# Kernel tuning notes

Measured on AMD Instinct MI355X. Metric: run time of the kernel, lower is better.

## Reference

```python
import jax, jax.numpy as jnp
import numpy as np

# dims
B, NO, NE = 32, 100, 600          # batch, img objects, img edges
NK, KE, L = 1000, 1000, 8         # kg entities, kg edges, token len
R = 8                              # reasoning-program nodes
H, IMG, LOC = 512, 2048, 5        # hidden, img feat, loc feat
EMB, V, MID, C = 300, 10000, 512, 3000
PAD = 1


def lang_encode(tokens, embed, W, b):
    # masked mean-pool of word embeddings + projection (LanguageEncoder)
    m = (tokens != PAD).astype(jnp.float32)            # [B,N,L]
    e = embed[tokens]                                   # [B,N,L,EMB]
    pooled = (e * m[..., None]).sum(-2) / jnp.maximum(m.sum(-1, keepdims=True), 1.0)
    return jnp.tanh(pooled @ W + b)                     # [B,N,H]


def find_attn(q, k, mask, Wq, Wk, v):
    # Find module: additive attention of program-node queries over key set
    qp = q @ Wq                                         # [B,R,MID]
    kp = k @ Wk                                         # [B,N,MID]
    s = jnp.einsum('brnm,m->brn', jnp.tanh(qp[:, :, None, :] + kp[:, None, :, :]), v)
    if mask is not None:
        s = jnp.where(mask[:, None, :], s, -1e9)
    return jax.nn.softmax(s, axis=-1)                   # [B,R,N] attention maps


def setup_inputs():
    key = jax.random.key(0)
    ks = jax.random.split(key, 30)
    w = lambda i, shp: jax.random.normal(ks[i], shp, jnp.float32) * 0.05
    inp = {
        'img_feat': jax.random.normal(ks[0], (B, NO, IMG), jnp.float32),
        'img_loc': jax.random.uniform(ks[1], (B, NO, LOC), jnp.float32),
        'img_node1_id_list': jax.random.randint(ks[2], (B, NE), 0, NO),
        'img_node2_id_list': jax.random.randint(ks[3], (B, NE), 0, NO),
        'kg_entity': jax.random.randint(ks[4], (B, NK, L), 0, V),
        'kg_e1_ids_list': jax.random.randint(ks[5], (B, KE), 0, NK),
        'kg_e2_ids_list': jax.random.randint(ks[6], (B, KE), 0, NK),
        'kg_edge': jax.random.randint(ks[7], (B, KE, L), 0, V),
        'r_nodes': jax.random.randint(ks[8], (B, R, L), 0, V),
        'r_connects': jax.random.randint(ks[9], (B, R), 0, R),
        'r_type': jax.random.randint(ks[10], (B, R), 0, 3),
        'embed': w(11, (V, EMB)),
        'W_lang': w(12, (EMB, H)), 'b_lang': jnp.zeros((H,), jnp.float32),
        'W_img': w(13, (IMG, H)), 'b_img': jnp.zeros((H,), jnp.float32),
        'W_loc': w(14, (LOC, H)), 'b_loc': jnp.zeros((H,), jnp.float32),
        'W_rel': w(15, (2 * H, H)), 'b_rel': jnp.zeros((H,), jnp.float32),
        'Wq_n': w(16, (H, MID)), 'Wk_n': w(17, (H, MID)), 'v_n': w(18, (MID,)),
        'Wq_e': w(19, (H, MID)), 'Wk_e': w(20, (H, MID)), 'v_e': w(21, (MID,)),
        'W1': w(22, (H, MID)), 'b1': jnp.zeros((MID,), jnp.float32),
        'W2': w(23, (MID, C)), 'b2': jnp.zeros((C,), jnp.float32),
    }
    return inp


def reference(img_feat, img_loc, img_node1_id_list, img_node2_id_list, kg_entity,
              kg_e1_ids_list, kg_e2_ids_list, kg_edge, r_nodes, r_connects, r_type,
              embed, W_lang, b_lang, W_img, b_img, W_loc, b_loc, W_rel, b_rel,
              Wq_n, Wk_n, v_n, Wq_e, Wk_e, v_e, W1, b1, W2, b2):
    # --- image graph features ---
    img_f = img_feat @ W_img + b_img                    # [B,NO,H]
    img_node_feat = img_f + (img_loc @ W_loc + b_loc)
    n1 = jnp.take_along_axis(img_f, img_node1_id_list[..., None], axis=1)  # [B,NE,H]
    n2 = jnp.take_along_axis(img_f, img_node2_id_list[..., None], axis=1)
    img_edge_feat = jnp.concatenate([n1, n2], -1) @ W_rel + b_rel          # [B,NE,H]
    # --- kg graph features ---
    kg_node_feat = lang_encode(kg_entity, embed, W_lang, b_lang)           # [B,NK,H]
    kg_node_mask = jnp.any(kg_entity != PAD, axis=-1)                      # [B,NK]
    kg_edge_feat = lang_encode(kg_edge, embed, W_lang, b_lang)             # [B,KE,H]
    # --- reasoning-program node features ---
    r_feat = lang_encode(r_nodes, embed, W_lang, b_lang)                   # [B,R,H]
    # --- Find over nodes (img + kg entities) ---
    node_keys = jnp.concatenate([img_node_feat, kg_node_feat], axis=1)     # [B,NO+NK,H]
    node_mask = jnp.concatenate([jnp.ones((B, NO), bool), kg_node_mask], axis=1)
    all_map = find_attn(r_feat, node_keys, node_mask, Wq_n, Wk_n, v_n)     # [B,R,NO+NK]
    node_re = jnp.einsum('brn,bnh->brh', all_map, node_keys)               # grounded node feats
    # --- Find over edges (img + kg relations) ---
    edge_keys = jnp.concatenate([img_edge_feat, kg_edge_feat], axis=1)     # [B,NE+KE,H]
    edge_map = find_attn(r_feat, edge_keys, None, Wq_e, Wk_e, v_e)
    edge_ctx = jnp.einsum('brn,bnh->brh', edge_map, edge_keys)
    # --- Reason head on root program node ---
    final = node_re[:, -1] + edge_ctx[:, -1]                               # [B,H]
    return jnp.tanh(final @ W1 + b1) @ W2 + b2                             # [B,C]
```

## Files before the change

kernel.cpp:

```cpp
#include <hip/hip_runtime.h>
#include <hip/hip_bf16.h>
#include <math.h>

#define B_   32
#define NO_  100
#define NE_  600
#define NK_  1000
#define KE_  1000
#define L_   8
#define R_   8
#define H_   512
#define IMG_ 2048
#define LOC_ 5
#define EMB_ 300
#define MID_ 512
#define C_   3000
#define PAD_ 1

#define NN_  (NO_ + NK_)
#define NEK_ (NE_ + KE_)

typedef __attribute__((ext_vector_type(8))) short bf16x8;
typedef __attribute__((ext_vector_type(4))) float f32x4;

__device__ __forceinline__ float4 ldf4(const float* p) { return *(const float4*)p; }

__device__ __forceinline__ float bf2f(short s) {
    unsigned u = ((unsigned)(unsigned short)s) << 16;
    float f; __builtin_memcpy(&f, &u, 4); return f;
}
__device__ __forceinline__ short f2bf(float f) {
    unsigned u; __builtin_memcpy(&u, &f, 4);
    u = (u + 0x7fffu + ((u >> 16) & 1u)) >> 16;
    return (short)u;
}

__device__ __forceinline__ void gload16(const void* g, void* l) {
    __builtin_amdgcn_global_load_lds(
        (__attribute__((address_space(1))) void*)(g),
        (__attribute__((address_space(3))) void*)(l), 16, 0, 0);
}

__global__ __launch_bounds__(256) void wprep_kernel(
    const float* __restrict__ W, short* __restrict__ Wp, int K, int KS)
{
    int idx = blockIdx.x * 256 + threadIdx.x;
    int total = 4 * KS * 4 * 128;
    if (idx >= total) return;
    int nl = idx & 127;
    int kg = (idx >> 7) & 3;
    int t  = idx >> 9;
    int ks = t % KS;
    int nb = t / KS;
    int n = nb * 128 + nl;
    short o[8];
#pragma unroll
    for (int j = 0; j < 8; ++j) {
        int k = ks * 32 + kg * 8 + j;
        o[j] = (k < K) ? f2bf(W[(long)k * H_ + n]) : (short)0;
    }
    *(uint4*)&Wp[(long)idx * 8] = *(uint4*)o;
}

__global__ __launch_bounds__(256) void cvt_bf16_kernel(
    const float* __restrict__ src, short* __restrict__ dst, long n)
{
    long i = ((long)blockIdx.x * 256 + threadIdx.x) * 8;
    if (i >= n) return;
    float4 a = ldf4(src + i), b = ldf4(src + i + 4);
    short o[8] = { f2bf(a.x), f2bf(a.y), f2bf(a.z), f2bf(a.w),
                   f2bf(b.x), f2bf(b.y), f2bf(b.z), f2bf(b.w) };
    *(uint4*)&dst[i] = *(uint4*)o;
}

__global__ __launch_bounds__(256) void pool_kernel(
    const int* __restrict__ tokens, int tok_stride, int tok_off,
    const short* __restrict__ embed_bf, short* __restrict__ pooled,
    float* __restrict__ maskout, int nrows)
{
    __shared__ int   toks[32][8];
    __shared__ float rinv[32];
    int tid = threadIdx.x, base = blockIdx.x * 32;
    {
        int r = tid >> 3, t = tid & 7;
        int i = base + r;
        toks[r][t] = (i < nrows) ? tokens[tok_off + (long)i * tok_stride + t] : PAD_;
    }
    __syncthreads();
    if (tid < 32) {
        int c = 0;
#pragma unroll
        for (int t = 0; t < 8; ++t) c += (toks[tid][t] != PAD_);
        rinv[tid] = 1.0f / fmaxf((float)c, 1.0f);
        int i = base + tid;
        if (maskout && i < nrows) maskout[i] = (c > 0) ? 1.0f : 0.0f;
    }
    __syncthreads();

    for (int task = tid; task < 32 * 40; task += 256) {
        int r = task / 40, kg = task - r * 40;
        float s[8] = {0.f,0.f,0.f,0.f,0.f,0.f,0.f,0.f};
        if (kg < 38) {
#pragma unroll
            for (int t = 0; t < 8; ++t) {
                int tok = toks[r][t];
                if (tok != PAD_) {
                    bf16x8 e = *(const bf16x8*)&embed_bf[(long)tok * EMB_ + kg * 8];
#pragma unroll
                    for (int j = 0; j < 8; ++j) s[j] += bf2f(e[j]);
                }
            }
        }
        float iv = rinv[r];
        short o[8];
#pragma unroll
        for (int j = 0; j < 8; ++j) {
            float v = s[j] * iv;
            if (kg == 37 && j >= 4) v = 0.f;
            o[j] = f2bf(v);
        }
        *(uint4*)&pooled[(long)(base + r) * 320 + kg * 8] = *(uint4*)o;
    }
}

template<int OUTF32>
__global__ __launch_bounds__(256) void keys_gemm_kernel(
    const short* __restrict__ A, const short* __restrict__ Wp,
    const float* __restrict__ bias,
    void* __restrict__ out, int rows_per_b, long out_bstride, long out_roff,
    int nrows)
{
    const int KS = 10;
    __shared__ __align__(16) short As[2 * 4096];
    __shared__ __align__(16) short Bs[2 * 4096];
    int tid = threadIdx.x;
    int m0 = blockIdx.x * 128, nb = blockIdx.y, n0 = nb * 128;
    int w = tid >> 6, l = tid & 63, wr = w >> 1, wc = w & 1;
    const short* wslab = Wp + (long)nb * KS * 4096;

    auto stage = [&](int buf, int ks) {
        short* Ad = As + buf * 4096 + w * 1024;
        short* Bd = Bs + buf * 4096 + w * 1024;
        const short* bsrc = wslab + (long)ks * 4096 + w * 1024 + l * 8;
#pragma unroll
        for (int i = 0; i < 2; ++i) {
            const short* ga = A + (long)(m0 + i * 64 + l) * 320 + ks * 32 + w * 8;
            gload16(ga, Ad + i * 512);
            gload16(bsrc + i * 512, Bd + i * 512);
        }
    };

    f32x4 acc[4][4];
#pragma unroll
    for (int m = 0; m < 4; ++m)
#pragma unroll
        for (int n = 0; n < 4; ++n)
#pragma unroll
            for (int k = 0; k < 4; ++k) acc[m][n][k] = 0.f;

    int kg = l >> 4, li = l & 15;
    stage(0, 0);
    __syncthreads();
    int buf = 0;
    for (int ks = 0; ks < KS; ++ks) {
        if (ks + 1 < KS) stage(buf ^ 1, ks + 1);
        bf16x8 af[4], bfr[4];
#pragma unroll
        for (int m = 0; m < 4; ++m)
            af[m] = *(const bf16x8*)&As[buf * 4096 + kg * 1024 + (wr * 64 + m * 16 + li) * 8];
#pragma unroll
        for (int n = 0; n < 4; ++n)
            bfr[n] = *(const bf16x8*)&Bs[buf * 4096 + kg * 1024 + (wc * 64 + n * 16 + li) * 8];
#pragma unroll
        for (int m = 0; m < 4; ++m)
#pragma unroll
            for (int n = 0; n < 4; ++n)
                acc[m][n] = __builtin_amdgcn_mfma_f32_16x16x32_bf16(af[m], bfr[n], acc[m][n], 0, 0, 0);
        __syncthreads();
        buf ^= 1;
    }

    int jrow4 = (l >> 4) * 4;
    float bv[4];
#pragma unroll
    for (int n = 0; n < 4; ++n) bv[n] = bias[n0 + wc * 64 + n * 16 + li];
#pragma unroll
    for (int m = 0; m < 4; ++m)
#pragma unroll
        for (int j = 0; j < 4; ++j) {
            int i = m0 + wr * 64 + m * 16 + jrow4 + j;
            if (i >= nrows) continue;
            int b = i / rows_per_b, k = i - b * rows_per_b;
#pragma unroll
            for (int n = 0; n < 4; ++n) {
                int col = n0 + wc * 64 + n * 16 + li;
                float val = tanhf(acc[m][n][j] + bv[n]);
                long idx = (long)b * out_bstride + out_roff + (long)k * H_ + col;
                if (OUTF32) ((float*)out)[idx] = val;
                else        ((short*)out)[idx] = f2bf(val);
            }
        }
}

template<int AV, int EP, int KS>
__global__ __launch_bounds__(256) void mfma_gemm_kernel(
    const short* __restrict__ A, int lda, const short* __restrict__ Wp,
    const int* __restrict__ id1, const int* __restrict__ id2,
    const short* __restrict__ Agather,
    const float* __restrict__ bias, const float* __restrict__ bias2,
    const float* __restrict__ loc, const float* __restrict__ Wloc,
    const float* __restrict__ qp, const float* __restrict__ vvec,
    short* __restrict__ out0, short* __restrict__ out1,
    float* __restrict__ sout, int Nrows, int Mtot)
{
    __shared__ __align__(16) short As[2 * 4096];
    __shared__ __align__(16) short Bs[2 * 4096];
    int tid = threadIdx.x;
    int m0 = blockIdx.x * 128, nb = blockIdx.y, n0 = nb * 128;
    int w = tid >> 6, l = tid & 63, wr = w >> 1, wc = w & 1;

    int r1[2], r2[2];
    if (AV == 2) {
#pragma unroll
        for (int i = 0; i < 2; ++i) {
            int row = m0 + i * 64 + l;
            int b = row / NE_;
            r1[i] = b * NO_ + id1[row];
            r2[i] = b * NO_ + id2[row];
        }
    }
    const short* wslab = Wp + (long)nb * KS * 4096;

    auto stage = [&](int buf, int ks) {
        short* Ad = As + buf * 4096 + w * 1024;
        short* Bd = Bs + buf * 4096 + w * 1024;
        const short* bsrc = wslab + (long)ks * 4096 + w * 1024 + l * 8;
#pragma unroll
        for (int i = 0; i < 2; ++i) {
            const short* ga;
            if (AV == 0) {
                ga = A + (long)(m0 + i * 64 + l) * lda + ks * 32 + w * 8;
            } else {
                int kk = ks * 32;
                int row = (kk < 512) ? r1[i] : r2[i];
                ga = Agather + (long)row * 512 + (kk & 511) + w * 8;
            }
            gload16(ga, Ad + i * 512);
            gload16(bsrc + i * 512, Bd + i * 512);
        }
    };

    f32x4 acc[4][4];
#pragma unroll
    for (int m = 0; m < 4; ++m)
#pragma unroll
        for (int n = 0; n < 4; ++n)
#pragma unroll
            for (int k = 0; k < 4; ++k) acc[m][n][k] = 0.f;

    int kg = l >> 4, li = l & 15;
    stage(0, 0);
    __syncthreads();
    int buf = 0;
    for (int ks = 0; ks < KS; ++ks) {
        if (ks + 1 < KS) stage(buf ^ 1, ks + 1);
        bf16x8 af[4], bfr[4];
#pragma unroll
        for (int m = 0; m < 4; ++m)
            af[m] = *(const bf16x8*)&As[buf * 4096 + kg * 1024 + (wr * 64 + m * 16 + li) * 8];
#pragma unroll
        for (int n = 0; n < 4; ++n)
            bfr[n] = *(const bf16x8*)&Bs[buf * 4096 + kg * 1024 + (wc * 64 + n * 16 + li) * 8];
#pragma unroll
        for (int m = 0; m < 4; ++m)
#pragma unroll
            for (int n = 0; n < 4; ++n)
                acc[m][n] = __builtin_amdgcn_mfma_f32_16x16x32_bf16(af[m], bfr[n], acc[m][n], 0, 0, 0);
        __syncthreads();
        buf ^= 1;
    }

    int jrow4 = (l >> 4) * 4;
    if (EP == 0) {
        float bi[4], bl[4], wl[4][5];
#pragma unroll
        for (int n = 0; n < 4; ++n) {
            int col = n0 + wc * 64 + n * 16 + li;
            bi[n] = bias[col]; bl[n] = bias2[col];
#pragma unroll
            for (int j5 = 0; j5 < 5; ++j5) wl[n][j5] = Wloc[j5 * H_ + col];
        }
#pragma unroll
        for (int m = 0; m < 4; ++m)
#pragma unroll
            for (int j = 0; j < 4; ++j) {
                int row = m0 + wr * 64 + m * 16 + jrow4 + j;
                int b = row / NO_, o = row - b * NO_;
                float lv[5];
#pragma unroll
                for (int j5 = 0; j5 < 5; ++j5) lv[j5] = loc[(long)row * 5 + j5];
#pragma unroll
                for (int n = 0; n < 4; ++n) {
                    int col = n0 + wc * 64 + n * 16 + li;
                    float val = acc[m][n][j] + bi[n];
                    out0[(long)row * H_ + col] = f2bf(val);
                    float nk = val + bl[n];
#pragma unroll
                    for (int j5 = 0; j5 < 5; ++j5) nk = fmaf(lv[j5], wl[n][j5], nk);
                    out1[((long)b * NN_ + o) * H_ + col] = f2bf(nk);
                }
            }
    } else if (EP == 1) {
        float bi[4];
#pragma unroll
        for (int n = 0; n < 4; ++n) bi[n] = bias[n0 + wc * 64 + n * 16 + li];
#pragma unroll
        for (int m = 0; m < 4; ++m)
#pragma unroll
            for (int j = 0; j < 4; ++j) {
                int row = m0 + wr * 64 + m * 16 + jrow4 + j;
                int b = row / NE_, e = row - b * NE_;
#pragma unroll
                for (int n = 0; n < 4; ++n) {
                    int col = n0 + wc * 64 + n * 16 + li;
                    out0[((long)b * NEK_ + e) * H_ + col] = f2bf(acc[m][n][j] + bi[n]);
                }
            }
    } else {
        float vv[4];
        int cols[4];
#pragma unroll
        for (int n = 0; n < 4; ++n) {
            cols[n] = n0 + wc * 64 + n * 16 + li;
            vv[n] = vvec[cols[n]];
        }
        int slot = nb * 2 + wc;
#pragma unroll
        for (int m = 0; m < 4; ++m)
#pragma unroll
            for (int j = 0; j < 4; ++j) {
                int row = m0 + wr * 64 + m * 16 + jrow4 + j;
                int b = row / Nrows;
                const float* qpb = qp + (long)b * H_;
                float p = 0.f;
#pragma unroll
                for (int n = 0; n < 4; ++n)
                    p += tanhf(qpb[cols[n]] + acc[m][n][j]) * vv[n];
                p += __shfl_xor(p, 1); p += __shfl_xor(p, 2);
                p += __shfl_xor(p, 4); p += __shfl_xor(p, 8);
                if (li == 0) sout[(long)slot * Mtot + row] = p;
            }
    }
}

__global__ __launch_bounds__(256) void softmax_w_kernel(
    const float* __restrict__ sp_n, const float* __restrict__ sp_e,
    const float* __restrict__ maskbuf, float* __restrict__ wn, float* __restrict__ we)
{
    __shared__ float sw[NEK_];
    __shared__ float red[256];
    int b = blockIdx.x, tid = threadIdx.x, set = blockIdx.y;
    const float* sp = set ? sp_e : sp_n;
    float* wout = set ? we : wn;
    int N = set ? NEK_ : NN_;
    long Mtot = set ? (long)B_ * NEK_ : (long)B_ * NN_;

    float lmax = -3.0e38f;
    for (int n = tid; n < N; n += 256) {
        long row = (long)b * N + n;
        float x = 0.f;
#pragma unroll
        for (int s = 0; s < 8; ++s) x += sp[(long)s * Mtot + row];
        if (!set && n >= NO_ && maskbuf[(long)b * NK_ + (n - NO_)] == 0.f) x = -1e30f;
        sw[n] = x;
        lmax = fmaxf(lmax, x);
    }
    red[tid] = lmax; __syncthreads();
    for (int st = 128; st > 0; st >>= 1) {
        if (tid < st) red[tid] = fmaxf(red[tid], red[tid + st]);
        __syncthreads();
    }
    float mx = red[0]; __syncthreads();

    float lsum = 0.f;
    for (int n = tid; n < N; n += 256) {
        float e = expf(sw[n] - mx);
        sw[n] = e;
        lsum += e;
    }
    red[tid] = lsum; __syncthreads();
    for (int st = 128; st > 0; st >>= 1) {
        if (tid < st) red[tid] += red[tid + st];
        __syncthreads();
    }
    float invZ = 1.0f / red[0];
    __syncthreads();
    for (int n = tid; n < N; n += 256)
        wout[(long)b * N + n] = sw[n] * invZ;
}

template<int SP>
__global__ __launch_bounds__(256) void wsum_kernel(
    const float* __restrict__ w, const short* __restrict__ keys,
    float* __restrict__ partial, int N)
{
    __shared__ float red[4][512];
    int b = blockIdx.x, sp = blockIdx.y, tid = threadIdx.x;
    int c8 = (tid & 63) * 8, rsub = tid >> 6;
    int per = (N + SP - 1) / SP;
    int n0 = sp * per, n1 = min(n0 + per, N);
    float acc[8] = {0.f,0.f,0.f,0.f,0.f,0.f,0.f,0.f};
    for (int n = n0 + rsub; n < n1; n += 4) {
        float wv = w[(long)b * N + n];
        bf16x8 k = *(const bf16x8*)&keys[((long)b * N + n) * H_ + c8];
#pragma unroll
        for (int j = 0; j < 8; ++j) acc[j] = fmaf(wv, bf2f(k[j]), acc[j]);
    }
    *(float4*)&red[rsub][c8]     = *(float4*)acc;
    *(float4*)&red[rsub][c8 + 4] = *(float4*)(acc + 4);
    __syncthreads();
    if (rsub == 0) {
        float o[8];
#pragma unroll
        for (int j = 0; j < 8; ++j)
            o[j] = red[0][c8 + j] + red[1][c8 + j] + red[2][c8 + j] + red[3][c8 + j];
        float* op = &partial[((long)sp * B_ + b) * H_ + c8];
        *(float4*)op       = *(float4*)o;
        *(float4*)(op + 4) = *(float4*)(o + 4);
    }
}

__global__ __launch_bounds__(256) void fin_reduce_kernel(
    const float* __restrict__ pn, const float* __restrict__ pe, float* __restrict__ fin)
{
    int i = blockIdx.x * 256 + threadIdx.x;
    float s = 0.f;
#pragma unroll
    for (int sp = 0; sp < 16; ++sp)
        s += pn[(long)sp * B_ * H_ + i] + pe[(long)sp * B_ * H_ + i];
    fin[i] = s;
}

template<int E, int CHUNK>
__global__ __launch_bounds__(256) void kmatvec_kernel(
    const float* __restrict__ in, const float* __restrict__ Wa,
    const float* __restrict__ Wb, float* __restrict__ pa,
    float* __restrict__ pb, int C)
{
    __shared__ float ins[32 * CHUNK];
    int tid = threadIdx.x;
    int ks = blockIdx.y, k0 = ks * CHUNK;
    const float* W   = (blockIdx.z == 0) ? Wa : Wb;
    float* partial   = (blockIdx.z == 0) ? pa : pb;
    for (int t = tid; t < 32 * CHUNK; t += 256) {
        int b = t / CHUNK, k = t - b * CHUNK;
        ins[t] = in[(long)b * E + k0 + k];
    }
    __syncthreads();
    int c = blockIdx.x * 256 + tid;
    if (c >= C) return;
    float acc[32];
#pragma unroll
    for (int b = 0; b < 32; ++b) acc[b] = 0.f;
    for (int k = 0; k < CHUNK; ++k) {
        float wv = W[(long)(k0 + k) * C + c];
#pragma unroll
        for (int b = 0; b < 32; ++b)
            acc[b] = fmaf(ins[b * CHUNK + k], wv, acc[b]);
    }
#pragma unroll
    for (int b = 0; b < 32; ++b)
        partial[((long)ks * 32 + b) * C + c] = acc[b];
}

template<int ACT, int KS>
__global__ __launch_bounds__(256) void kreduce_kernel(
    const float* __restrict__ pa, const float* __restrict__ pb,
    const float* __restrict__ biasa, const float* __restrict__ biasb,
    float* __restrict__ oa, float* __restrict__ ob, int C)
{
    int set = blockIdx.y;
    const float* p    = set ? pb : pa;
    const float* bias = set ? biasb : biasa;
    float* o          = set ? ob : oa;
    long i = (long)blockIdx.x * 256 + threadIdx.x;
    if (i >= 32L * C) return;
    int c = (int)(i % C);
    float s = bias ? bias[c] : 0.f;
#pragma unroll
    for (int ks = 0; ks < KS; ++ks) s += p[(long)ks * 32 * C + i];
    o[i] = (ACT == 1) ? tanhf(s) : s;
}

extern "C" void kernel_launch(void* const* d_in, const int* in_sizes, int n_in,
                              void* d_out, int out_size, void* d_ws, size_t ws_size,
                              hipStream_t stream)
{
    (void)in_sizes; (void)n_in; (void)out_size; (void)ws_size;

    const float* img_feat  = (const float*)d_in[0];
    const float* img_loc   = (const float*)d_in[1];
    const int*   id1       = (const int*)d_in[2];
    const int*   id2       = (const int*)d_in[3];
    const int*   kg_entity = (const int*)d_in[4];
    const int*   kg_edge   = (const int*)d_in[7];
    const int*   r_nodes   = (const int*)d_in[8];
    const float* embed     = (const float*)d_in[11];
    const float* W_lang    = (const float*)d_in[12];
    const float* b_lang    = (const float*)d_in[13];
    const float* W_img     = (const float*)d_in[14];
    const float* b_img     = (const float*)d_in[15];
    const float* W_loc     = (const float*)d_in[16];
    const float* b_loc     = (const float*)d_in[17];
    const float* W_rel     = (const float*)d_in[18];
    const float* b_rel     = (const float*)d_in[19];
    const float* Wq_n      = (const float*)d_in[20];
    const float* Wk_n      = (const float*)d_in[21];
    const float* v_n       = (const float*)d_in[22];
    const float* Wq_e      = (const float*)d_in[23];
    const float* Wk_e      = (const float*)d_in[24];
    const float* v_e       = (const float*)d_in[25];
    const float* W1        = (const float*)d_in[26];
    const float* b1        = (const float*)d_in[27];
    const float* W2        = (const float*)d_in[28];
    const float* b2        = (const float*)d_in[29];
    float* out = (float*)d_out;

    char* ws = (char*)d_ws;
    size_t off = 0;
    auto allocS = [&](size_t n) { short* p = (short*)(ws + off); off += ((n * 2 + 255) & ~255ULL); return p; };
    auto allocF = [&](size_t n) { float* p = (float*)(ws + off); off += ((n * 4 + 255) & ~255ULL); return p; };

    short* img_feat_bf = allocS((size_t)B_ * NO_ * IMG_);
    short* embed_bf    = allocS((size_t)10000 * EMB_ + 16);
    short* Wp_img      = allocS((size_t)4 * 64 * 4096);
    short* Wp_rel      = allocS((size_t)4 * 32 * 4096);
    short* Wp_kn       = allocS((size_t)4 * 16 * 4096);
    short* Wp_ke       = allocS((size_t)4 * 16 * 4096);
    short* Wp_lang     = allocS((size_t)4 * 10 * 4096);
    short* img_f_bf    = allocS((size_t)B_ * NO_ * H_);
    short* node_keys   = allocS((size_t)B_ * NN_ * H_);
    short* edge_keys   = allocS((size_t)B_ * NEK_ * H_);
    short* pooled_n    = allocS((size_t)B_ * NK_ * 320);
    short* pooled_e    = allocS((size_t)B_ * KE_ * 320);
    short* pooled_r    = allocS((size_t)128 * 320);
    float* rfeat   = allocF((size_t)B_ * H_);
    float* qp_n    = allocF((size_t)B_ * H_);
    float* qp_e    = allocF((size_t)B_ * H_);
    float* mask_kg = allocF((size_t)B_ * NK_);
    float* sp_n    = allocF((size_t)8 * B_ * NN_);
    float* sp_e    = allocF((size_t)8 * B_ * NEK_);
    float* wn      = allocF((size_t)B_ * NN_);
    float* we      = allocF((size_t)B_ * NEK_);
    float* pn      = allocF((size_t)16 * B_ * H_);
    float* pe      = allocF((size_t)16 * B_ * H_);
    float* fin     = allocF((size_t)B_ * H_);
    float* hid     = allocF((size_t)B_ * H_);
    float* pq_n    = allocF((size_t)16 * B_ * MID_);
    float* pq_e    = allocF((size_t)16 * B_ * MID_);
    float* ph1     = allocF((size_t)16 * B_ * MID_);
    float* ph2     = allocF((size_t)16 * B_ * C_);

    cvt_bf16_kernel<<<(B_ * NO_ * IMG_ / 8 + 255) / 256, 256, 0, stream>>>(
        img_feat, img_feat_bf, (long)B_ * NO_ * IMG_);
    cvt_bf16_kernel<<<(10000 * EMB_ / 8 + 255) / 256, 256, 0, stream>>>(
        embed, embed_bf, (long)10000 * EMB_);
    wprep_kernel<<<512, 256, 0, stream>>>(W_img,  Wp_img,  IMG_, 64);
    wprep_kernel<<<256, 256, 0, stream>>>(W_rel,  Wp_rel,  1024, 32);
    wprep_kernel<<<128, 256, 0, stream>>>(Wk_n,   Wp_kn,   512,  16);
    wprep_kernel<<<128, 256, 0, stream>>>(Wk_e,   Wp_ke,   512,  16);
    wprep_kernel<<< 80, 256, 0, stream>>>(W_lang, Wp_lang, EMB_, 10);

    pool_kernel<<<B_ * NK_ / 32, 256, 0, stream>>>(
        kg_entity, L_, 0, embed_bf, pooled_n, mask_kg, B_ * NK_);
    pool_kernel<<<B_ * KE_ / 32, 256, 0, stream>>>(
        kg_edge, L_, 0, embed_bf, pooled_e, nullptr, B_ * KE_);
    pool_kernel<<<4, 256, 0, stream>>>(
        r_nodes, R_ * L_, (R_ - 1) * L_, embed_bf, pooled_r, nullptr, B_);

    keys_gemm_kernel<0><<<dim3(B_ * NK_ / 128, 4), 256, 0, stream>>>(
        pooled_n, Wp_lang, b_lang, node_keys, NK_, (long)NN_ * H_, (long)NO_ * H_,
        B_ * NK_);
    keys_gemm_kernel<0><<<dim3(B_ * KE_ / 128, 4), 256, 0, stream>>>(
        pooled_e, Wp_lang, b_lang, edge_keys, KE_, (long)NEK_ * H_, (long)NE_ * H_,
        B_ * KE_);
    keys_gemm_kernel<1><<<dim3(1, 4), 256, 0, stream>>>(
        pooled_r, Wp_lang, b_lang, rfeat, 1, (long)H_, 0L, B_);

    kmatvec_kernel<H_, 32><<<dim3(2, 16, 2), 256, 0, stream>>>(
        rfeat, Wq_n, Wq_e, pq_n, pq_e, MID_);
    kreduce_kernel<0, 16><<<dim3(B_ * MID_ / 256, 2), 256, 0, stream>>>(
        pq_n, pq_e, nullptr, nullptr, qp_n, qp_e, MID_);

    mfma_gemm_kernel<0, 0, 64><<<dim3(B_ * NO_ / 128, 4), 256, 0, stream>>>(
        img_feat_bf, IMG_, Wp_img, nullptr, nullptr, nullptr,
        b_img, b_loc, img_loc, W_loc, nullptr, nullptr,
        img_f_bf, node_keys, nullptr, 0, 0);
    mfma_gemm_kernel<2, 1, 32><<<dim3(B_ * NE_ / 128, 4), 256, 0, stream>>>(
        nullptr, 0, Wp_rel, id1, id2, img_f_bf,
        b_rel, nullptr, nullptr, nullptr, nullptr, nullptr,
        edge_keys, nullptr, nullptr, 0, 0);

    mfma_gemm_kernel<0, 2, 16><<<dim3(B_ * NN_ / 128, 4), 256, 0, stream>>>(
        node_keys, H_, Wp_kn, nullptr, nullptr, nullptr,
        nullptr, nullptr, nullptr, nullptr, qp_n, v_n,
        nullptr, nullptr, sp_n, NN_, B_ * NN_);
    mfma_gemm_kernel<0, 2, 16><<<dim3(B_ * NEK_ / 128, 4), 256, 0, stream>>>(
        edge_keys, H_, Wp_ke, nullptr, nullptr, nullptr,
        nullptr, nullptr, nullptr, nullptr, qp_e, v_e,
        nullptr, nullptr, sp_e, NEK_, B_ * NEK_);

    softmax_w_kernel<<<dim3(B_, 2), 256, 0, stream>>>(sp_n, sp_e, mask_kg, wn, we);
    wsum_kernel<16><<<dim3(B_, 16), 256, 0, stream>>>(wn, node_keys, pn, NN_);
    wsum_kernel<16><<<dim3(B_, 16), 256, 0, stream>>>(we, edge_keys, pe, NEK_);
    fin_reduce_kernel<<<B_ * H_ / 256, 256, 0, stream>>>(pn, pe, fin);

    kmatvec_kernel<H_, 32><<<dim3(2, 16, 1), 256, 0, stream>>>(
        fin, W1, W1, ph1, ph1, MID_);
    kreduce_kernel<1, 16><<<dim3(B_ * MID_ / 256, 1), 256, 0, stream>>>(
        ph1, ph1, b1, b1, hid, hid, MID_);
    kmatvec_kernel<MID_, 32><<<dim3((C_ + 255) / 256, 16, 1), 256, 0, stream>>>(
        hid, W2, W2, ph2, ph2, C_);
    kreduce_kernel<0, 16><<<dim3((B_ * C_ + 255) / 256, 1), 256, 0, stream>>>(
        ph2, ph2, b2, b2, out, out, C_);
}
```

Measured before the change: 516.3 us.

## Merge kg entity/edge pooling and key GEMMs; use 64-wide K chunks without double buffering

Fuses the kg-entity and kg-edge pooling launches into one launch and the two language-key GEMMs into one dual-output GEMM, so fewer kernels run and each grid is larger. All MFMA GEMMs now stage a 64-wide K chunk per barrier pair (two MFMA sub-steps) into a single buffer instead of double-buffering 32-wide chunks. This halves the number of barriers and loop iterations but drops the overlap between global loads and compute.

```diff
diff --git a/kernel.cpp b/kernel.cpp
--- a/kernel.cpp
+++ b/kernel.cpp
@@ -74,17 +74,20 @@
 }
 
 __global__ __launch_bounds__(256) void pool_kernel(
-    const int* __restrict__ tokens, int tok_stride, int tok_off,
-    const short* __restrict__ embed_bf, short* __restrict__ pooled,
-    float* __restrict__ maskout, int nrows)
+    const int* __restrict__ tokA, const int* __restrict__ tokB, int split,
+    int tok_stride, int tok_off, const short* __restrict__ embed_bf,
+    short* __restrict__ pooled, float* __restrict__ maskout, int nrows)
 {
     __shared__ int   toks[32][8];
     __shared__ float rinv[32];
     int tid = threadIdx.x, base = blockIdx.x * 32;
+    const int* tokens; int local;
+    if (base < split) { tokens = tokA; local = base; }
+    else              { tokens = tokB; local = base - split; }
     {
         int r = tid >> 3, t = tid & 7;
         int i = base + r;
-        toks[r][t] = (i < nrows) ? tokens[tok_off + (long)i * tok_stride + t] : PAD_;
+        toks[r][t] = (i < nrows) ? tokens[tok_off + (long)(local + r) * tok_stride + t] : PAD_;
     }
     __syncthreads();
     if (tid < 32) {
@@ -93,7 +96,7 @@
         for (int t = 0; t < 8; ++t) c += (toks[tid][t] != PAD_);
         rinv[tid] = 1.0f / fmaxf((float)c, 1.0f);
         int i = base + tid;
-        if (maskout && i < nrows) maskout[i] = (c > 0) ? 1.0f : 0.0f;
+        if (maskout && i < split && i < nrows) maskout[i] = (c > 0) ? 1.0f : 0.0f;
     }
     __syncthreads();
 
@@ -123,32 +126,19 @@
     }
 }
 
-template<int OUTF32>
+template<int DUAL, int OUTF32>
 __global__ __launch_bounds__(256) void keys_gemm_kernel(
     const short* __restrict__ A, const short* __restrict__ Wp,
     const float* __restrict__ bias,
-    void* __restrict__ out, int rows_per_b, long out_bstride, long out_roff,
-    int nrows)
-{
-    const int KS = 10;
-    __shared__ __align__(16) short As[2 * 4096];
-    __shared__ __align__(16) short Bs[2 * 4096];
+    void* __restrict__ outA, short* __restrict__ outB, int nrows)
+{
+    const int NCH = 5;
+    __shared__ __align__(16) short As[8192];
+    __shared__ __align__(16) short Bs[8192];
     int tid = threadIdx.x;
     int m0 = blockIdx.x * 128, nb = blockIdx.y, n0 = nb * 128;
     int w = tid >> 6, l = tid & 63, wr = w >> 1, wc = w & 1;
-    const short* wslab = Wp + (long)nb * KS * 4096;
-
-    auto stage = [&](int buf, int ks) {
-        short* Ad = As + buf * 4096 + w * 1024;
-        short* Bd = Bs + buf * 4096 + w * 1024;
-        const short* bsrc = wslab + (long)ks * 4096 + w * 1024 + l * 8;
-#pragma unroll
-        for (int i = 0; i < 2; ++i) {
-            const short* ga = A + (long)(m0 + i * 64 + l) * 320 + ks * 32 + w * 8;
-            gload16(ga, Ad + i * 512);
-            gload16(bsrc + i * 512, Bd + i * 512);
-        }
-    };
+    const short* wslab = Wp + (long)nb * (NCH * 2) * 4096;
 
     f32x4 acc[4][4];
 #pragma unroll
@@ -159,25 +149,32 @@
             for (int k = 0; k < 4; ++k) acc[m][n][k] = 0.f;
 
     int kg = l >> 4, li = l & 15;
-    stage(0, 0);
-    __syncthreads();
-    int buf = 0;
-    for (int ks = 0; ks < KS; ++ks) {
-        if (ks + 1 < KS) stage(buf ^ 1, ks + 1);
-        bf16x8 af[4], bfr[4];
-#pragma unroll
-        for (int m = 0; m < 4; ++m)
-            af[m] = *(const bf16x8*)&As[buf * 4096 + kg * 1024 + (wr * 64 + m * 16 + li) * 8];
-#pragma unroll
-        for (int n = 0; n < 4; ++n)
-            bfr[n] = *(const bf16x8*)&Bs[buf * 4096 + kg * 1024 + (wc * 64 + n * 16 + li) * 8];
-#pragma unroll
-        for (int m = 0; m < 4; ++m)
+    for (int t = 0; t < NCH; ++t) {
+#pragma unroll
+        for (int j = 0; j < 4; ++j) {
+            int c = w * 4 + j;
+            int g = c >> 1, h2 = c & 1;
+            const short* ga = A + (long)(m0 + h2 * 64 + l) * 320 + t * 64 + g * 8;
+            gload16(ga, As + c * 512);
+            gload16(wslab + ((long)t * 2) * 4096 + c * 512 + l * 8, Bs + c * 512);
+        }
+        __syncthreads();
+#pragma unroll
+        for (int s = 0; s < 2; ++s) {
+            bf16x8 af[4], bfr[4];
+#pragma unroll
+            for (int m = 0; m < 4; ++m)
+                af[m] = *(const bf16x8*)&As[(s * 4 + kg) * 1024 + (wr * 64 + m * 16 + li) * 8];
 #pragma unroll
             for (int n = 0; n < 4; ++n)
-                acc[m][n] = __builtin_amdgcn_mfma_f32_16x16x32_bf16(af[m], bfr[n], acc[m][n], 0, 0, 0);
+                bfr[n] = *(const bf16x8*)&Bs[(s * 4 + kg) * 1024 + (wc * 64 + n * 16 + li) * 8];
+#pragma unroll
+            for (int m = 0; m < 4; ++m)
+#pragma unroll
+                for (int n = 0; n < 4; ++n)
+                    acc[m][n] = __builtin_amdgcn_mfma_f32_16x16x32_bf16(af[m], bfr[n], acc[m][n], 0, 0, 0);
+        }
         __syncthreads();
-        buf ^= 1;
     }
 
     int jrow4 = (l >> 4) * 4;
@@ -190,19 +187,29 @@
         for (int j = 0; j < 4; ++j) {
             int i = m0 + wr * 64 + m * 16 + jrow4 + j;
             if (i >= nrows) continue;
-            int b = i / rows_per_b, k = i - b * rows_per_b;
 #pragma unroll
             for (int n = 0; n < 4; ++n) {
                 int col = n0 + wc * 64 + n * 16 + li;
                 float val = tanhf(acc[m][n][j] + bv[n]);
-                long idx = (long)b * out_bstride + out_roff + (long)k * H_ + col;
-                if (OUTF32) ((float*)out)[idx] = val;
-                else        ((short*)out)[idx] = f2bf(val);
+                if (DUAL) {
+                    if (i < B_ * NK_) {
+                        int b = i / NK_, k = i - b * NK_;
+                        ((short*)outA)[(long)b * (NN_ * H_) + (long)(NO_ + k) * H_ + col] = f2bf(val);
+                    } else {
+                        int i2 = i - B_ * NK_;
+                        int b = i2 / KE_, k = i2 - b * KE_;
+                        outB[(long)b * (NEK_ * H_) + (long)(NE_ + k) * H_ + col] = f2bf(val);
+                    }
+                } else {
+                    long idx = (long)i * H_ + col;
+                    if (OUTF32) ((float*)outA)[idx] = val;
+                    else        ((short*)outA)[idx] = f2bf(val);
+                }
             }
         }
 }
 
-template<int AV, int EP, int KS>
+template<int AV, int EP, int NCH>
 __global__ __launch_bounds__(256) void mfma_gemm_kernel(
     const short* __restrict__ A, int lda, const short* __restrict__ Wp,
     const int* __restrict__ id1, const int* __restrict__ id2,
@@ -213,8 +220,8 @@
     short* __restrict__ out0, short* __restrict__ out1,
     float* __restrict__ sout, int Nrows, int Mtot)
 {
-    __shared__ __align__(16) short As[2 * 4096];
-    __shared__ __align__(16) short Bs[2 * 4096];
+    __shared__ __align__(16) short As[8192];
+    __shared__ __align__(16) short Bs[8192];
     int tid = threadIdx.x;
     int m0 = blockIdx.x * 128, nb = blockIdx.y, n0 = nb * 128;
     int w = tid >> 6, l = tid & 63, wr = w >> 1, wc = w & 1;
@@ -229,55 +236,50 @@
             r2[i] = b * NO_ + id2[row];
         }
     }
-    const short* wslab = Wp + (long)nb * KS * 4096;
-
-    auto stage = [&](int buf, int ks) {
-        short* Ad = As + buf * 4096 + w * 1024;
-        short* Bd = Bs + buf * 4096 + w * 1024;
-        const short* bsrc = wslab + (long)ks * 4096 + w * 1024 + l * 8;
-#pragma unroll
-        for (int i = 0; i < 2; ++i) {
+    const short* wslab = Wp + (long)nb * (NCH * 2) * 4096;
+
+    f32x4 acc[4][4];
+#pragma unroll
+    for (int m = 0; m < 4; ++m)
+#pragma unroll
+        for (int n = 0; n < 4; ++n)
+#pragma unroll
+            for (int k = 0; k < 4; ++k) acc[m][n][k] = 0.f;
+
+    int kg = l >> 4, li = l & 15;
+    for (int t = 0; t < NCH; ++t) {
+#pragma unroll
+        for (int j = 0; j < 4; ++j) {
+            int c = w * 4 + j;
+            int g = c >> 1, h2 = c & 1;
             const short* ga;
             if (AV == 0) {
-                ga = A + (long)(m0 + i * 64 + l) * lda + ks * 32 + w * 8;
+                ga = A + (long)(m0 + h2 * 64 + l) * lda + t * 64 + g * 8;
             } else {
-                int kk = ks * 32;
-                int row = (kk < 512) ? r1[i] : r2[i];
-                ga = Agather + (long)row * 512 + (kk & 511) + w * 8;
+                int kk = t * 64 + g * 8;
+                int row = (kk < 512) ? r1[h2] : r2[h2];
+                ga = Agather + (long)row * 512 + (kk & 511);
             }
-            gload16(ga, Ad + i * 512);
-            gload16(bsrc + i * 512, Bd + i * 512);
-        }
-    };
-
-    f32x4 acc[4][4];
-#pragma unroll
-    for (int m = 0; m < 4; ++m)
-#pragma unroll
-        for (int n = 0; n < 4; ++n)
-#pragma unroll
-            for (int k = 0; k < 4; ++k) acc[m][n][k] = 0.f;
-
-    int kg = l >> 4, li = l & 15;
-    stage(0, 0);
-    __syncthreads();
-    int buf = 0;
-    for (int ks = 0; ks < KS; ++ks) {
-        if (ks + 1 < KS) stage(buf ^ 1, ks + 1);
-        bf16x8 af[4], bfr[4];
-#pragma unroll
-        for (int m = 0; m < 4; ++m)
-            af[m] = *(const bf16x8*)&As[buf * 4096 + kg * 1024 + (wr * 64 + m * 16 + li) * 8];
-#pragma unroll
-        for (int n = 0; n < 4; ++n)
-            bfr[n] = *(const bf16x8*)&Bs[buf * 4096 + kg * 1024 + (wc * 64 + n * 16 + li) * 8];
-#pragma unroll
-        for (int m = 0; m < 4; ++m)
+            gload16(ga, As + c * 512);
+            gload16(wslab + ((long)t * 2) * 4096 + c * 512 + l * 8, Bs + c * 512);
+        }
+        __syncthreads();
+#pragma unroll
+        for (int s = 0; s < 2; ++s) {
+            bf16x8 af[4], bfr[4];
+#pragma unroll
+            for (int m = 0; m < 4; ++m)
+                af[m] = *(const bf16x8*)&As[(s * 4 + kg) * 1024 + (wr * 64 + m * 16 + li) * 8];
 #pragma unroll
             for (int n = 0; n < 4; ++n)
-                acc[m][n] = __builtin_amdgcn_mfma_f32_16x16x32_bf16(af[m], bfr[n], acc[m][n], 0, 0, 0);
+                bfr[n] = *(const bf16x8*)&Bs[(s * 4 + kg) * 1024 + (wc * 64 + n * 16 + li) * 8];
+#pragma unroll
+            for (int m = 0; m < 4; ++m)
+#pragma unroll
+                for (int n = 0; n < 4; ++n)
+                    acc[m][n] = __builtin_amdgcn_mfma_f32_16x16x32_bf16(af[m], bfr[n], acc[m][n], 0, 0, 0);
+        }
         __syncthreads();
-        buf ^= 1;
     }
 
     int jrow4 = (l >> 4) * 4;
@@ -541,8 +543,7 @@
     short* img_f_bf    = allocS((size_t)B_ * NO_ * H_);
     short* node_keys   = allocS((size_t)B_ * NN_ * H_);
     short* edge_keys   = allocS((size_t)B_ * NEK_ * H_);
-    short* pooled_n    = allocS((size_t)B_ * NK_ * 320);
-    short* pooled_e    = allocS((size_t)B_ * KE_ * 320);
+    short* pooled      = allocS((size_t)2 * B_ * NK_ * 320);
     short* pooled_r    = allocS((size_t)128 * 320);
     float* rfeat   = allocF((size_t)B_ * H_);
     float* qp_n    = allocF((size_t)B_ * H_);
@@ -571,41 +572,36 @@
     wprep_kernel<<<128, 256, 0, stream>>>(Wk_e,   Wp_ke,   512,  16);
     wprep_kernel<<< 80, 256, 0, stream>>>(W_lang, Wp_lang, EMB_, 10);
 
-    pool_kernel<<<B_ * NK_ / 32, 256, 0, stream>>>(
-        kg_entity, L_, 0, embed_bf, pooled_n, mask_kg, B_ * NK_);
-    pool_kernel<<<B_ * KE_ / 32, 256, 0, stream>>>(
-        kg_edge, L_, 0, embed_bf, pooled_e, nullptr, B_ * KE_);
+    pool_kernel<<<2 * B_ * NK_ / 32, 256, 0, stream>>>(
+        kg_entity, kg_edge, B_ * NK_, L_, 0, embed_bf, pooled, mask_kg, 2 * B_ * NK_);
     pool_kernel<<<4, 256, 0, stream>>>(
-        r_nodes, R_ * L_, (R_ - 1) * L_, embed_bf, pooled_r, nullptr, B_);
-
-    keys_gemm_kernel<0><<<dim3(B_ * NK_ / 128, 4), 256, 0, stream>>>(
-        pooled_n, Wp_lang, b_lang, node_keys, NK_, (long)NN_ * H_, (long)NO_ * H_,
-        B_ * NK_);
-    keys_gemm_kernel<0><<<dim3(B_ * KE_ / 128, 4), 256, 0, stream>>>(
-        pooled_e, Wp_lang, b_lang, edge_keys, KE_, (long)NEK_ * H_, (long)NE_ * H_,
-        B_ * KE_);
-    keys_gemm_kernel<1><<<dim3(1, 4), 256, 0, stream>>>(
-        pooled_r, Wp_lang, b_lang, rfeat, 1, (long)H_, 0L, B_);
+        r_nodes, nullptr, 1 << 30, R_ * L_, (R_ - 1) * L_, embed_bf, pooled_r,
+        nullptr, B_);
+
+    keys_gemm_kernel<1, 0><<<dim3(2 * B_ * NK_ / 128, 4), 256, 0, stream>>>(
+        pooled, Wp_lang, b_lang, node_keys, edge_keys, 2 * B_ * NK_);
+    keys_gemm_kernel<0, 1><<<dim3(1, 4), 256, 0, stream>>>(
+        pooled_r, Wp_lang, b_lang, rfeat, nullptr, B_);
 
     kmatvec_kernel<H_, 32><<<dim3(2, 16, 2), 256, 0, stream>>>(
         rfeat, Wq_n, Wq_e, pq_n, pq_e, MID_);
     kreduce_kernel<0, 16><<<dim3(B_ * MID_ / 256, 2), 256, 0, stream>>>(
         pq_n, pq_e, nullptr, nullptr, qp_n, qp_e, MID_);
 
-    mfma_gemm_kernel<0, 0, 64><<<dim3(B_ * NO_ / 128, 4), 256, 0, stream>>>(
+    mfma_gemm_kernel<0, 0, 32><<<dim3(B_ * NO_ / 128, 4), 256, 0, stream>>>(
         img_feat_bf, IMG_, Wp_img, nullptr, nullptr, nullptr,
         b_img, b_loc, img_loc, W_loc, nullptr, nullptr,
         img_f_bf, node_keys, nullptr, 0, 0);
-    mfma_gemm_kernel<2, 1, 32><<<dim3(B_ * NE_ / 128, 4), 256, 0, stream>>>(
+    mfma_gemm_kernel<2, 1, 16><<<dim3(B_ * NE_ / 128, 4), 256, 0, stream>>>(
         nullptr, 0, Wp_rel, id1, id2, img_f_bf,
         b_rel, nullptr, nullptr, nullptr, nullptr, nullptr,
         edge_keys, nullptr, nullptr, 0, 0);
 
-    mfma_gemm_kernel<0, 2, 16><<<dim3(B_ * NN_ / 128, 4), 256, 0, stream>>>(
+    mfma_gemm_kernel<0, 2, 8><<<dim3(B_ * NN_ / 128, 4), 256, 0, stream>>>(
         node_keys, H_, Wp_kn, nullptr, nullptr, nullptr,
         nullptr, nullptr, nullptr, nullptr, qp_n, v_n,
         nullptr, nullptr, sp_n, NN_, B_ * NN_);
-    mfma_gemm_kernel<0, 2, 16><<<dim3(B_ * NEK_ / 128, 4), 256, 0, stream>>>(
+    mfma_gemm_kernel<0, 2, 8><<<dim3(B_ * NEK_ / 128, 4), 256, 0, stream>>>(
         edge_keys, H_, Wp_ke, nullptr, nullptr, nullptr,
         nullptr, nullptr, nullptr, nullptr, qp_e, v_e,
         nullptr, nullptr, sp_e, NEK_, B_ * NEK_);
```

After: 448.1 us. -13.2%, faster.
